# Performance work log

Measured on AMD Instinct MI355X. Metric: run time of the kernel, lower is better.

## Reference

```python
import jax, jax.numpy as jnp
import numpy as np

TEMPERATURE = 0.01
STRIDE = 16  # original image coords -> feature grid (1024 / 64)


def setup_inputs() -> dict:
    key = jax.random.key(0)
    k1, k2, k3, k4, k5 = jax.random.split(key, 5)
    B, C, Hf, Wf, N = 32, 256, 64, 64, 64
    feats_src = jax.random.normal(k1, (B, C, Hf, Wf), dtype=jnp.float32)
    feats_trg = jax.random.normal(k2, (B, C, Hf, Wf), dtype=jnp.float32)
    # keypoints in original-image coordinates [0, 1024)
    kps_src = jax.random.uniform(k3, (B, N, 2), dtype=jnp.float32) * 1024.0
    kps_trg = jax.random.uniform(k4, (B, N, 2), dtype=jnp.float32) * 1024.0
    kps_mask = jax.random.bernoulli(k5, 0.7, (B, N))
    return {"feats_src": feats_src, "feats_trg": feats_trg,
            "kps_src": kps_src, "kps_trg": kps_trg, "kps_mask": kps_mask}


def _l2_normalize(x):
    # F.normalize(x, dim=1): x / max(||x||_2, eps)
    n = jnp.linalg.norm(x, axis=1, keepdims=True)
    return x / jnp.maximum(n, 1e-12)


def _kps_to_flat_idx(kps, Hf, Wf):
    # int(coord/16) truncation (coords >= 0 so trunc == floor), then clamp.
    fx = jnp.clip((kps[..., 0] / STRIDE).astype(jnp.int32), 0, Wf - 1)
    fy = jnp.clip((kps[..., 1] / STRIDE).astype(jnp.int32), 0, Hf - 1)
    return fy * Wf + fx  # (B, N)


def reference(feats_src, feats_trg, kps_src, kps_trg, kps_mask):
    B, C, Hf, Wf = feats_src.shape
    fs = _l2_normalize(feats_src).reshape(B, C, Hf * Wf)
    ft = _l2_normalize(feats_trg).reshape(B, C, Hf * Wf)

    src_idx = _kps_to_flat_idx(kps_src, Hf, Wf)  # (B, N)
    trg_idx = _kps_to_flat_idx(kps_trg, Hf, Wf)  # (B, N)

    # Gather query vectors at source keypoint cells: (B, C, N)
    queries = jnp.take_along_axis(fs, src_idx[:, None, :], axis=2)
    # Batched logits over all target cells: (B, N, Hf*Wf)
    logits = jnp.einsum('bcn,bcm->bnm', queries, ft) / TEMPERATURE

    logp = jax.nn.log_softmax(logits, axis=-1)
    nll = -jnp.take_along_axis(logp, trg_idx[..., None], axis=-1)[..., 0]  # (B, N)

    m = kps_mask.astype(nll.dtype)
    count = jnp.sum(m)
    # Masked mean over valid keypoints; 0 if no valid keypoints (matches torch).
    return jnp.sum(nll * m) / jnp.maximum(count, 1.0)
```

## Files before the change

### kernel.cpp

```cpp
#include <hip/hip_runtime.h>
#include <hip/hip_fp16.h>
#include <cstdint>

#define BB 32
#define CC 256
#define HF 64
#define WF 64
#define MM 4096
#define NN 64
#define MCHUNKS 32
#define MPB 128
#define KSTEPS 8
#define NBLK (BB * MCHUNKS)

typedef _Float16 half8 __attribute__((ext_vector_type(8)));
typedef __fp16 fp16x2 __attribute__((ext_vector_type(2)));
typedef float f32x4 __attribute__((ext_vector_type(4)));


__global__ void phase0_gather_norm(const float* __restrict__ fs,
                                   const float* __restrict__ kps_src,
                                   const float* __restrict__ kps_trg,
                                   const void* __restrict__ maskp,
                                   _Float16* __restrict__ wq,
                                   int* __restrict__ trgidx,
                                   float* __restrict__ minfoF,
                                   int* __restrict__ minfoI,
                                   float* __restrict__ out) {
  int blk = blockIdx.x;
  int b = blk >> 6, n = blk & 63;
  int c = threadIdx.x;

  float kx = kps_src[blk * 2 + 0];
  float ky = kps_src[blk * 2 + 1];
  int fx = min(max((int)(kx * (1.0f / 16.0f)), 0), WF - 1);
  int fy = min(max((int)(ky * (1.0f / 16.0f)), 0), HF - 1);
  int pix = fy * WF + fx;

  float x = fs[((size_t)b * CC + c) * MM + pix];

  float v = x * x;
  #pragma unroll
  for (int off = 32; off >= 1; off >>= 1) v += __shfl_xor(v, off);
  __shared__ float ssum[4];
  int wid = c >> 6, lane = c & 63;
  if (lane == 0) ssum[wid] = v;
  __syncthreads();
  float tot = ssum[0] + ssum[1] + ssum[2] + ssum[3];
  float inv = 1.0f / fmaxf(sqrtf(tot), 1e-12f);

  int ks = c >> 5, kg = (c >> 3) & 3, j = c & 7;
  int nt = n >> 4, nr = n & 15;
  int lane_f = kg * 16 + nr;
  size_t off = (size_t)b * 16384 + (size_t)((ks * 4 + nt) * 64 + lane_f) * 8 + j;
  wq[off] = (_Float16)(x * inv);

  if (c == 0) {
    float tx = kps_trg[blk * 2 + 0], ty = kps_trg[blk * 2 + 1];
    int gx = min(max((int)(tx * (1.0f / 16.0f)), 0), WF - 1);
    int gy = min(max((int)(ty * (1.0f / 16.0f)), 0), HF - 1);
    trgidx[blk] = gy * WF + gx;
  }

  if (blk == 0) {
    __shared__ int flagF, flagB;
    if (c == 0) { flagF = 0; flagB = 0; out[0] = 0.0f; }
    __syncthreads();
    const unsigned char* mb = (const unsigned char*)maskp;
    int lf = 0, lb = 0;
    for (int i = c; i < BB * NN; i += 256) {
      unsigned char vch = mb[i];
      int r = i & 3;
      if (r == 3 && vch == 0x3F) lf = 1;
      if (r != 0 && vch != 0) lb = 1;
    }
    if (lf) atomicOr(&flagF, 1);
    if (lb) atomicOr(&flagB, 1);
    __syncthreads();
    int layout = flagF ? 2 : (flagB ? 0 : 1);

    float lc = 0.f;
    for (int i = c; i < BB * NN; i += 256) {
      float mval;
      if (layout == 2) mval = ((const float*)maskp)[i];
      else if (layout == 0) mval = (float)mb[i];
      else mval = (float)((const int*)maskp)[i];
      lc += mval;
    }
    #pragma unroll
    for (int o2 = 32; o2 >= 1; o2 >>= 1) lc += __shfl_xor(lc, o2);
    __shared__ float cs[4];
    if (lane == 0) cs[wid] = lc;
    __syncthreads();
    if (c == 0) {
      minfoF[0] = cs[0] + cs[1] + cs[2] + cs[3];
      minfoI[1] = layout;
    }
  }
}

__global__ void __launch_bounds__(256, 4)
phaseB(const float* __restrict__ ft,
       const _Float16* __restrict__ wq,
       const int* __restrict__ tidx,
       float* __restrict__ partM,
       float* __restrict__ partS,
       float* __restrict__ trgl) {
  __shared__ _Float16 qf[16384];
  __shared__ int trg_lds[NN];
  __shared__ float pM[4 * NN], pS[4 * NN];

  int b = blockIdx.x >> 5, mc = blockIdx.x & 31;
  int tid = threadIdx.x;

  const uint4* src = (const uint4*)(wq + (size_t)b * 16384);
  uint4* dst = (uint4*)qf;
  #pragma unroll
  for (int i = 0; i < 8; ++i) dst[tid + 256 * i] = src[tid + 256 * i];
  if (tid < NN) trg_lds[tid] = tidx[b * NN + tid];
  __syncthreads();

  int w = tid >> 6, lane = tid & 63, g = lane >> 4, col = lane & 15;
  int m0 = mc * MPB + w * 32;
  const float* fb = ft + (size_t)b * CC * MM;
  const float* lb0 = fb + (size_t)(g * 8) * MM + (m0 + col);
  const float* lb1 = lb0 + 16;

  f32x4 acc[4][2];
  #pragma unroll
  for (int nt = 0; nt < 4; ++nt)
    #pragma unroll
    for (int mt = 0; mt < 2; ++mt) acc[nt][mt] = (f32x4){0.f, 0.f, 0.f, 0.f};
  float ss0 = 0.f, ss1 = 0.f;

  const half8* qv = (const half8*)qf;

  float cur0[8], cur1[8], nxt0[8], nxt1[8];
  #pragma unroll
  for (int j = 0; j < 8; ++j) {
    cur0[j] = lb0[(size_t)j * MM];
    cur1[j] = lb1[(size_t)j * MM];
  }

  #pragma unroll
  for (int ks = 0; ks < KSTEPS; ++ks) {
    if (ks + 1 < KSTEPS) {
      #pragma unroll
      for (int j = 0; j < 8; ++j) {
        nxt0[j] = lb0[(size_t)((ks + 1) * 32 + j) * MM];
        nxt1[j] = lb1[(size_t)((ks + 1) * 32 + j) * MM];
      }
    }

    half8 a0 = qv[(ks * 4 + 0) * 64 + lane];
    half8 a1 = qv[(ks * 4 + 1) * 64 + lane];
    half8 a2 = qv[(ks * 4 + 2) * 64 + lane];
    half8 a3 = qv[(ks * 4 + 3) * 64 + lane];

    half8 b0, b1;
    #pragma unroll
    for (int j = 0; j < 4; ++j) {
      ss0 += cur0[2 * j] * cur0[2 * j] + cur0[2 * j + 1] * cur0[2 * j + 1];
      ss1 += cur1[2 * j] * cur1[2 * j] + cur1[2 * j + 1] * cur1[2 * j + 1];
      fp16x2 h0 = __builtin_amdgcn_cvt_pkrtz(cur0[2 * j], cur0[2 * j + 1]);
      fp16x2 h1 = __builtin_amdgcn_cvt_pkrtz(cur1[2 * j], cur1[2 * j + 1]);
      b0[2 * j] = (_Float16)h0[0]; b0[2 * j + 1] = (_Float16)h0[1];
      b1[2 * j] = (_Float16)h1[0]; b1[2 * j + 1] = (_Float16)h1[1];
    }

    acc[0][0] = __builtin_amdgcn_mfma_f32_16x16x32_f16(b0, a0, acc[0][0], 0, 0, 0);
    acc[1][0] = __builtin_amdgcn_mfma_f32_16x16x32_f16(b0, a1, acc[1][0], 0, 0, 0);
    acc[2][0] = __builtin_amdgcn_mfma_f32_16x16x32_f16(b0, a2, acc[2][0], 0, 0, 0);
    acc[3][0] = __builtin_amdgcn_mfma_f32_16x16x32_f16(b0, a3, acc[3][0], 0, 0, 0);
    acc[0][1] = __builtin_amdgcn_mfma_f32_16x16x32_f16(b1, a0, acc[0][1], 0, 0, 0);
    acc[1][1] = __builtin_amdgcn_mfma_f32_16x16x32_f16(b1, a1, acc[1][1], 0, 0, 0);
    acc[2][1] = __builtin_amdgcn_mfma_f32_16x16x32_f16(b1, a2, acc[2][1], 0, 0, 0);
    acc[3][1] = __builtin_amdgcn_mfma_f32_16x16x32_f16(b1, a3, acc[3][1], 0, 0, 0);

    #pragma unroll
    for (int j = 0; j < 8; ++j) { cur0[j] = nxt0[j]; cur1[j] = nxt1[j]; }
  }

  ss0 += __shfl_xor(ss0, 16); ss0 += __shfl_xor(ss0, 32);
  ss1 += __shfl_xor(ss1, 16); ss1 += __shfl_xor(ss1, 32);

  float sc0[4], sc1[4];
  #pragma unroll
  for (int r = 0; r < 4; ++r) {
    float t0 = __shfl(ss0, g * 4 + r, 16);
    float t1 = __shfl(ss1, g * 4 + r, 16);
    sc0[r] = 100.0f / fmaxf(sqrtf(t0), 1e-12f);
    sc1[r] = 100.0f / fmaxf(sqrtf(t1), 1e-12f);
  }

  #pragma unroll
  for (int nt = 0; nt < 4; ++nt) {
    int n = nt * 16 + col;
    int t = trg_lds[n];
    float v[8];
    #pragma unroll
    for (int r = 0; r < 4; ++r) {
      v[r]     = acc[nt][0][r] * sc0[r];
      v[4 + r] = acc[nt][1][r] * sc1[r];
    }
    #pragma unroll
    for (int r = 0; r < 4; ++r) {
      if (t == m0 + g * 4 + r)      trgl[b * NN + n] = v[r];
      if (t == m0 + 16 + g * 4 + r) trgl[b * NN + n] = v[4 + r];
    }
    float mx = fmaxf(fmaxf(fmaxf(v[0], v[1]), fmaxf(v[2], v[3])),
                     fmaxf(fmaxf(v[4], v[5]), fmaxf(v[6], v[7])));
    mx = fmaxf(mx, __shfl_xor(mx, 16));
    mx = fmaxf(mx, __shfl_xor(mx, 32));
    float s = 0.f;
    #pragma unroll
    for (int j = 0; j < 8; ++j) s += __expf(v[j] - mx);
    s += __shfl_xor(s, 16);
    s += __shfl_xor(s, 32);
    if (g == 0) { pM[w * NN + n] = mx; pS[w * NN + n] = s; }
  }
  __syncthreads();

  if (tid < NN) {
    int n = tid;
    float gm = fmaxf(fmaxf(pM[n], pM[NN + n]), fmaxf(pM[2 * NN + n], pM[3 * NN + n]));
    float S = 0.f;
    #pragma unroll
    for (int ww = 0; ww < 4; ++ww)
      S += pS[ww * NN + n] * __expf(pM[ww * NN + n] - gm);
    partM[mc * (BB * NN) + b * NN + n] = gm;
    partS[mc * (BB * NN) + b * NN + n] = S;
  }
}

__global__ void __launch_bounds__(256)
reduceFinal(const float* __restrict__ partM,
            const float* __restrict__ partS,
            const float* __restrict__ trgl,
            const void* __restrict__ maskp,
            const float* __restrict__ minfoF,
            const int* __restrict__ minfoI,
            float* __restrict__ out) {
  int tid = threadIdx.x;
  int p = blockIdx.x * 256 + tid;

  float gm = -1e30f, S = 0.f;
  #pragma unroll
  for (int c2 = 0; c2 < MCHUNKS; ++c2) {
    float mi = partM[c2 * (BB * NN) + p];
    float si = partS[c2 * (BB * NN) + p];
    float nm = fmaxf(gm, mi);
    S = S * __expf(gm - nm) + si * __expf(mi - nm);
    gm = nm;
  }
  float nll = gm + logf(S) - trgl[p];

  int layout = minfoI[1];
  const unsigned char* mb = (const unsigned char*)maskp;
  float mval;
  if (layout == 2) mval = ((const float*)maskp)[p];
  else if (layout == 0) mval = (float)mb[p];
  else mval = (float)((const int*)maskp)[p];

  float v = nll * mval;
  #pragma unroll
  for (int off = 32; off >= 1; off >>= 1) v += __shfl_xor(v, off);
  __shared__ float ps[4];
  int w = tid >> 6, lane = tid & 63;
  if (lane == 0) ps[w] = v;
  __syncthreads();
  if (tid == 0) {
    float s = ps[0] + ps[1] + ps[2] + ps[3];
    float cnt = minfoF[0];
    atomicAdd(out, s / fmaxf(cnt, 1.0f));
  }
}

extern "C" void kernel_launch(void* const* d_in, const int* in_sizes, int n_in,
                              void* d_out, int out_size, void* d_ws, size_t ws_size,
                              hipStream_t stream) {
  const float* fs   = (const float*)d_in[0];
  const float* ft   = (const float*)d_in[1];
  const float* ksrc = (const float*)d_in[2];
  const float* ktrg = (const float*)d_in[3];
  const void*  mask = d_in[4];
  float* out = (float*)d_out;

  _Float16* wq = (_Float16*)d_ws;
  float* partM = (float*)((char*)d_ws + (size_t)BB * 16384 * 2);
  float* partS = partM + (size_t)MCHUNKS * BB * NN;
  float* trgl  = partS + (size_t)MCHUNKS * BB * NN;
  int* tidx    = (int*)(trgl + BB * NN);
  float* minfoF = (float*)(tidx + BB * NN);
  int* minfoI   = (int*)minfoF;

  phase0_gather_norm<<<BB * NN, 256, 0, stream>>>(fs, ksrc, ktrg, mask, wq, tidx,
                                                  minfoF, minfoI, out);
  phaseB<<<NBLK, 256, 0, stream>>>(ft, wq, tidx, partM, partS, trgl);
  reduceFinal<<<BB * NN / 256, 256, 0, stream>>>(partM, partS, trgl, mask,
                                                 minfoF, minfoI, out);
}
```

Measured before the change: 47.21 us.

## Widen phaseB tiles to 256 cells per block with float4 loads

Each wave now covers 64 target cells using float4 vector loads (4 MFMA column groups per lane) instead of 32 cells with scalar loads. The grid shrinks to 16 chunks per batch, which halves the redundant per-block copying of queries into LDS and the number of partial softmax results. The partial max/sum layout is transposed so the final reduction reads contiguous float4s. The trade-off is higher register use (occupancy hint dropped) and fewer blocks (512) available to hide memory latency.

```diff
diff --git a/kernel.cpp b/kernel.cpp
--- a/kernel.cpp
+++ b/kernel.cpp
@@ -8,8 +8,8 @@
 #define WF 64
 #define MM 4096
 #define NN 64
-#define MCHUNKS 32
-#define MPB 128
+#define MCHUNKS 16
+#define MPB 256
 #define KSTEPS 8
 #define NBLK (BB * MCHUNKS)
 
@@ -99,7 +99,7 @@
   }
 }
 
-__global__ void __launch_bounds__(256, 4)
+__global__ void __launch_bounds__(256)
 phaseB(const float* __restrict__ ft,
        const _Float16* __restrict__ wq,
        const int* __restrict__ tidx,
@@ -110,7 +110,7 @@
   __shared__ int trg_lds[NN];
   __shared__ float pM[4 * NN], pS[4 * NN];
 
-  int b = blockIdx.x >> 5, mc = blockIdx.x & 31;
+  int b = blockIdx.x >> 4, mc = blockIdx.x & 15;
   int tid = threadIdx.x;
 
   const uint4* src = (const uint4*)(wq + (size_t)b * 16384);
@@ -121,100 +121,105 @@
   __syncthreads();
 
   int w = tid >> 6, lane = tid & 63, g = lane >> 4, col = lane & 15;
-  int m0 = mc * MPB + w * 32;
+  int m0w = mc * MPB + w * 64;
   const float* fb = ft + (size_t)b * CC * MM;
-  const float* lb0 = fb + (size_t)(g * 8) * MM + (m0 + col);
-  const float* lb1 = lb0 + 16;
-
-  f32x4 acc[4][2];
-  #pragma unroll
-  for (int nt = 0; nt < 4; ++nt)
-    #pragma unroll
-    for (int mt = 0; mt < 2; ++mt) acc[nt][mt] = (f32x4){0.f, 0.f, 0.f, 0.f};
-  float ss0 = 0.f, ss1 = 0.f;
+  const float4* lb = (const float4*)(fb + (size_t)(g * 8) * MM + (m0w + 4 * col));
+  #define ROW4 (MM / 4)
+
+  f32x4 acc[4][4];
+  #pragma unroll
+  for (int jj = 0; jj < 4; ++jj)
+    #pragma unroll
+    for (int nt = 0; nt < 4; ++nt) acc[jj][nt] = (f32x4){0.f, 0.f, 0.f, 0.f};
+  float ssq[4] = {0.f, 0.f, 0.f, 0.f};
 
   const half8* qv = (const half8*)qf;
 
-  float cur0[8], cur1[8], nxt0[8], nxt1[8];
-  #pragma unroll
-  for (int j = 0; j < 8; ++j) {
-    cur0[j] = lb0[(size_t)j * MM];
-    cur1[j] = lb1[(size_t)j * MM];
-  }
+  float4 cur[8], nxt[8];
+  #pragma unroll
+  for (int j = 0; j < 8; ++j) cur[j] = lb[(size_t)j * ROW4];
 
   #pragma unroll
   for (int ks = 0; ks < KSTEPS; ++ks) {
     if (ks + 1 < KSTEPS) {
       #pragma unroll
-      for (int j = 0; j < 8; ++j) {
-        nxt0[j] = lb0[(size_t)((ks + 1) * 32 + j) * MM];
-        nxt1[j] = lb1[(size_t)((ks + 1) * 32 + j) * MM];
+      for (int j = 0; j < 8; ++j)
+        nxt[j] = lb[(size_t)((ks + 1) * 32 + j) * ROW4];
+    }
+
+    half8 qn0 = qv[(ks * 4 + 0) * 64 + lane];
+    half8 qn1 = qv[(ks * 4 + 1) * 64 + lane];
+    half8 qn2 = qv[(ks * 4 + 2) * 64 + lane];
+    half8 qn3 = qv[(ks * 4 + 3) * 64 + lane];
+
+    half8 aft[4];
+    #pragma unroll
+    for (int jj = 0; jj < 4; ++jj) {
+      #pragma unroll
+      for (int j = 0; j < 8; j += 2) {
+        float u0 = cur[j][jj], u1 = cur[j + 1][jj];
+        ssq[jj] += u0 * u0 + u1 * u1;
+        fp16x2 h = __builtin_amdgcn_cvt_pkrtz(u0, u1);
+        aft[jj][j] = (_Float16)h[0];
+        aft[jj][j + 1] = (_Float16)h[1];
       }
     }
 
-    half8 a0 = qv[(ks * 4 + 0) * 64 + lane];
-    half8 a1 = qv[(ks * 4 + 1) * 64 + lane];
-    half8 a2 = qv[(ks * 4 + 2) * 64 + lane];
-    half8 a3 = qv[(ks * 4 + 3) * 64 + lane];
-
-    half8 b0, b1;
-    #pragma unroll
-    for (int j = 0; j < 4; ++j) {
-      ss0 += cur0[2 * j] * cur0[2 * j] + cur0[2 * j + 1] * cur0[2 * j + 1];
-      ss1 += cur1[2 * j] * cur1[2 * j] + cur1[2 * j + 1] * cur1[2 * j + 1];
-      fp16x2 h0 = __builtin_amdgcn_cvt_pkrtz(cur0[2 * j], cur0[2 * j + 1]);
-      fp16x2 h1 = __builtin_amdgcn_cvt_pkrtz(cur1[2 * j], cur1[2 * j + 1]);
-      b0[2 * j] = (_Float16)h0[0]; b0[2 * j + 1] = (_Float16)h0[1];
-      b1[2 * j] = (_Float16)h1[0]; b1[2 * j + 1] = (_Float16)h1[1];
-    }
-
-    acc[0][0] = __builtin_amdgcn_mfma_f32_16x16x32_f16(b0, a0, acc[0][0], 0, 0, 0);
-    acc[1][0] = __builtin_amdgcn_mfma_f32_16x16x32_f16(b0, a1, acc[1][0], 0, 0, 0);
-    acc[2][0] = __builtin_amdgcn_mfma_f32_16x16x32_f16(b0, a2, acc[2][0], 0, 0, 0);
-    acc[3][0] = __builtin_amdgcn_mfma_f32_16x16x32_f16(b0, a3, acc[3][0], 0, 0, 0);
-    acc[0][1] = __builtin_amdgcn_mfma_f32_16x16x32_f16(b1, a0, acc[0][1], 0, 0, 0);
-    acc[1][1] = __builtin_amdgcn_mfma_f32_16x16x32_f16(b1, a1, acc[1][1], 0, 0, 0);
-    acc[2][1] = __builtin_amdgcn_mfma_f32_16x16x32_f16(b1, a2, acc[2][1], 0, 0, 0);
-    acc[3][1] = __builtin_amdgcn_mfma_f32_16x16x32_f16(b1, a3, acc[3][1], 0, 0, 0);
-
-    #pragma unroll
-    for (int j = 0; j < 8; ++j) { cur0[j] = nxt0[j]; cur1[j] = nxt1[j]; }
-  }
-
-  ss0 += __shfl_xor(ss0, 16); ss0 += __shfl_xor(ss0, 32);
-  ss1 += __shfl_xor(ss1, 16); ss1 += __shfl_xor(ss1, 32);
-
-  float sc0[4], sc1[4];
-  #pragma unroll
-  for (int r = 0; r < 4; ++r) {
-    float t0 = __shfl(ss0, g * 4 + r, 16);
-    float t1 = __shfl(ss1, g * 4 + r, 16);
-    sc0[r] = 100.0f / fmaxf(sqrtf(t0), 1e-12f);
-    sc1[r] = 100.0f / fmaxf(sqrtf(t1), 1e-12f);
-  }
+    #pragma unroll
+    for (int jj = 0; jj < 4; ++jj) {
+      acc[jj][0] = __builtin_amdgcn_mfma_f32_16x16x32_f16(aft[jj], qn0, acc[jj][0], 0, 0, 0);
+      acc[jj][1] = __builtin_amdgcn_mfma_f32_16x16x32_f16(aft[jj], qn1, acc[jj][1], 0, 0, 0);
+      acc[jj][2] = __builtin_amdgcn_mfma_f32_16x16x32_f16(aft[jj], qn2, acc[jj][2], 0, 0, 0);
+      acc[jj][3] = __builtin_amdgcn_mfma_f32_16x16x32_f16(aft[jj], qn3, acc[jj][3], 0, 0, 0);
+    }
+
+    #pragma unroll
+    for (int j = 0; j < 8; ++j) cur[j] = nxt[j];
+  }
+
+  #pragma unroll
+  for (int jj = 0; jj < 4; ++jj) {
+    ssq[jj] += __shfl_xor(ssq[jj], 16);
+    ssq[jj] += __shfl_xor(ssq[jj], 32);
+  }
+  float sc[4][4];
+  #pragma unroll
+  for (int jj = 0; jj < 4; ++jj)
+    #pragma unroll
+    for (int r = 0; r < 4; ++r) {
+      float t = __shfl(ssq[jj], 4 * g + r, 16);
+      sc[jj][r] = 100.0f / fmaxf(sqrtf(t), 1e-12f);
+    }
 
   #pragma unroll
   for (int nt = 0; nt < 4; ++nt) {
     int n = nt * 16 + col;
     int t = trg_lds[n];
-    float v[8];
-    #pragma unroll
-    for (int r = 0; r < 4; ++r) {
-      v[r]     = acc[nt][0][r] * sc0[r];
-      v[4 + r] = acc[nt][1][r] * sc1[r];
-    }
-    #pragma unroll
-    for (int r = 0; r < 4; ++r) {
-      if (t == m0 + g * 4 + r)      trgl[b * NN + n] = v[r];
-      if (t == m0 + 16 + g * 4 + r) trgl[b * NN + n] = v[4 + r];
-    }
-    float mx = fmaxf(fmaxf(fmaxf(v[0], v[1]), fmaxf(v[2], v[3])),
-                     fmaxf(fmaxf(v[4], v[5]), fmaxf(v[6], v[7])));
+    float v[4][4];
+    #pragma unroll
+    for (int jj = 0; jj < 4; ++jj)
+      #pragma unroll
+      for (int r = 0; r < 4; ++r)
+        v[jj][r] = acc[jj][nt][r] * sc[jj][r];
+
+    #pragma unroll
+    for (int jj = 0; jj < 4; ++jj)
+      #pragma unroll
+      for (int r = 0; r < 4; ++r)
+        if (t == m0w + 16 * g + 4 * r + jj) trgl[b * NN + n] = v[jj][r];
+
+    float mx = -1e30f;
+    #pragma unroll
+    for (int jj = 0; jj < 4; ++jj)
+      #pragma unroll
+      for (int r = 0; r < 4; ++r) mx = fmaxf(mx, v[jj][r]);
     mx = fmaxf(mx, __shfl_xor(mx, 16));
     mx = fmaxf(mx, __shfl_xor(mx, 32));
     float s = 0.f;
     #pragma unroll
-    for (int j = 0; j < 8; ++j) s += __expf(v[j] - mx);
+    for (int jj = 0; jj < 4; ++jj)
+      #pragma unroll
+      for (int r = 0; r < 4; ++r) s += __expf(v[jj][r] - mx);
     s += __shfl_xor(s, 16);
     s += __shfl_xor(s, 32);
     if (g == 0) { pM[w * NN + n] = mx; pS[w * NN + n] = s; }
@@ -228,8 +233,8 @@
     #pragma unroll
     for (int ww = 0; ww < 4; ++ww)
       S += pS[ww * NN + n] * __expf(pM[ww * NN + n] - gm);
-    partM[mc * (BB * NN) + b * NN + n] = gm;
-    partS[mc * (BB * NN) + b * NN + n] = S;
+    partM[(size_t)(b * NN + n) * MCHUNKS + mc] = gm;
+    partS[(size_t)(b * NN + n) * MCHUNKS + mc] = S;
   }
 }
 
@@ -244,14 +249,21 @@
   int tid = threadIdx.x;
   int p = blockIdx.x * 256 + tid;
 
+  const float4* pm4 = (const float4*)(partM + (size_t)p * MCHUNKS);
+  const float4* ps4 = (const float4*)(partS + (size_t)p * MCHUNKS);
   float gm = -1e30f, S = 0.f;
   #pragma unroll
-  for (int c2 = 0; c2 < MCHUNKS; ++c2) {
-    float mi = partM[c2 * (BB * NN) + p];
-    float si = partS[c2 * (BB * NN) + p];
-    float nm = fmaxf(gm, mi);
-    S = S * __expf(gm - nm) + si * __expf(mi - nm);
-    gm = nm;
+  for (int q = 0; q < MCHUNKS / 4; ++q) {
+    float4 m4 = pm4[q];
+    float4 s4 = ps4[q];
+    #pragma unroll
+    for (int e = 0; e < 4; ++e) {
+      float mi = ((const float*)&m4)[e];
+      float si = ((const float*)&s4)[e];
+      float nm = fmaxf(gm, mi);
+      S = S * __expf(gm - nm) + si * __expf(mi - nm);
+      gm = nm;
+    }
   }
   float nll = gm + logf(S) - trgl[p];
 
@@ -288,8 +300,8 @@
 
   _Float16* wq = (_Float16*)d_ws;
   float* partM = (float*)((char*)d_ws + (size_t)BB * 16384 * 2);
-  float* partS = partM + (size_t)MCHUNKS * BB * NN;
-  float* trgl  = partS + (size_t)MCHUNKS * BB * NN;
+  float* partS = partM + (size_t)BB * NN * MCHUNKS;
+  float* trgl  = partS + (size_t)BB * NN * MCHUNKS;
   int* tidx    = (int*)(trgl + BB * NN);
   float* minfoF = (float*)(tidx + BB * NN);
   int* minfoI   = (int*)minfoF;
```

New measurement: 54.07 us. 14.5% more time.
